# Kernel tuning notes

Measured on AMD Instinct MI355X. Metric: run time of the kernel, lower is better.

## Reference

```python
import jax, jax.numpy as jnp
import numpy as np

N, E, D, H = 50000, 800000, 128, 4

def setup_inputs() -> dict:
    key = jax.random.key(0)
    ks = jax.random.split(key, 6)
    x = jax.random.normal(ks[0], (N, D), dtype=jnp.float32)
    edge_index = jax.random.randint(ks[1], (2, E), 0, N, dtype=jnp.int64)
    W = jax.random.normal(ks[2], (D, H * D), dtype=jnp.float32) * (1.0 / np.sqrt(D))
    att_src = jax.random.normal(ks[3], (H, D), dtype=jnp.float32) * 0.1
    att_dst = jax.random.normal(ks[4], (H, D), dtype=jnp.float32) * 0.1
    bias = jnp.zeros((D,), dtype=jnp.float32)
    gamma = jnp.ones((D,), dtype=jnp.float32)
    beta = jnp.zeros((D,), dtype=jnp.float32)
    return {"x": x, "edge_index": edge_index, "W": W, "att_src": att_src,
            "att_dst": att_dst, "bias": bias, "gamma": gamma, "beta": beta}

def reference(x, edge_index, W, att_src, att_dst, bias, gamma, beta):
    src, dst = edge_index[0], edge_index[1]
    # GATConv: linear transform per head -> [N, H, D]
    xw = (x @ W).reshape(N, H, D)
    a_src = jnp.einsum('nhd,hd->nh', xw, att_src)  # [N, H]
    a_dst = jnp.einsum('nhd,hd->nh', xw, att_dst)  # [N, H]
    alpha = a_src[src] + a_dst[dst]                # [E, H]
    alpha = jax.nn.leaky_relu(alpha, negative_slope=0.2)
    # segment softmax over incoming edges of each dst node
    m = jax.ops.segment_max(alpha, dst, num_segments=N)   # [N, H]
    ex = jnp.exp(alpha - m[dst])                            # [E, H]
    denom = jax.ops.segment_sum(ex, dst, num_segments=N)   # [N, H]
    attn = ex / denom[dst]                                  # [E, H]
    msg = xw[src] * attn[:, :, None]                        # [E, H, D]
    agg = jax.ops.segment_sum(msg, dst, num_segments=N)    # [N, H, D]
    out = agg.mean(axis=1) + bias                           # concat=False: mean heads
    # LayerNorm (eps=1e-5)
    mu = out.mean(axis=-1, keepdims=True)
    var = out.var(axis=-1, keepdims=True)
    out = (out - mu) * jax.lax.rsqrt(var + 1e-5) * gamma + beta
    out = jax.nn.gelu(out, approximate=False)
    return out + x  # project is Identity (in_channels == out_channels)
```

## Files before the change

### kernel.cpp

```cpp
#include <hip/hip_runtime.h>
#include <hip/hip_bf16.h>
#include <hip/hip_fp16.h>
#include <math.h>

#define ND 128
#define NH 4
#define HD 512

typedef __attribute__((ext_vector_type(8))) short bf16x8;
typedef __attribute__((ext_vector_type(4))) float f32x4;
typedef __attribute__((ext_vector_type(2))) float f32x2;

__device__ __forceinline__ unsigned pack_bf16(float a, float b) {
    unsigned ua = __float_as_uint(a), ub = __float_as_uint(b);
    ua = (ua + 0x7fffu + ((ua >> 16) & 1u)) >> 16;
    ub = (ub + 0x7fffu + ((ub >> 16) & 1u)) >> 16;
    return ua | (ub << 16);
}
__device__ __forceinline__ unsigned short bf16r(float a) {
    unsigned ua = __float_as_uint(a);
    return (unsigned short)((ua + 0x7fffu + ((ua >> 16) & 1u)) >> 16);
}
__device__ __forceinline__ float bflo(unsigned u) { return __uint_as_float(u << 16); }
__device__ __forceinline__ float bfhi(unsigned u) { return __uint_as_float(u & 0xffff0000u); }
__device__ __forceinline__ unsigned pack_half2(float a, float b) {
    __half ha = __float2half(a), hb = __float2half(b);
    return (unsigned)__half_as_ushort(ha) | ((unsigned)__half_as_ushort(hb) << 16);
}
__device__ __forceinline__ float2 h22f(unsigned u) {
    __half2 h = *(__half2*)&u;
    return __half22float2(h);
}

__global__ __launch_bounds__(256) void prep_misc(const float* __restrict__ W,
                                                 const float* __restrict__ att_src,
                                                 const float* __restrict__ att_dst,
                                                 unsigned short* __restrict__ Ws,
                                                 float* __restrict__ pt,
                                                 const int* __restrict__ dst,
                                                 int* __restrict__ cnt, int ne) {
    int b = blockIdx.x;
    if (b < 16) {
        __shared__ float tile[64][65];
        int h = b >> 2, rt = (b >> 1) & 1, ct = b & 1;
        int tx = threadIdx.x;
        int rr = tx >> 6, c = tx & 63;
#pragma unroll
        for (int i = 0; i < 16; ++i) {
            int r = i * 4 + rr;
            tile[r][c] = W[(size_t)(rt * 64 + r) * HD + h * ND + ct * 64 + c];
        }
        __syncthreads();
#pragma unroll
        for (int i = 0; i < 16; ++i) {
            int r = i * 4 + rr;
            Ws[(size_t)(ct * 64 + r) * HD + h * ND + rt * 64 + c] = bf16r(tile[c][r]);
        }
    } else if (b < 48) {
        int w = threadIdx.x >> 6, lane = threadIdx.x & 63;
        int k = (b - 16) * 4 + w;
#pragma unroll
        for (int h = 0; h < NH; ++h) {
            float2 wv = ((const float2*)(W + (size_t)k * HD + h * ND))[lane];
            float2 as = ((const float2*)(att_src + h * ND))[lane];
            float2 ad = ((const float2*)(att_dst + h * ND))[lane];
            float ps = wv.x * as.x + wv.y * as.y;
            float pd = wv.x * ad.x + wv.y * ad.y;
#pragma unroll
            for (int off = 1; off < 64; off <<= 1) {
                ps += __shfl_xor(ps, off);
                pd += __shfl_xor(pd, off);
            }
            if (lane == 0) {
                pt[h * ND + k] = ps;
                pt[(4 + h) * ND + k] = pd;
            }
        }
    } else {
        int e = (b - 48) * 256 + threadIdx.x;
        if (e < ne) atomicAdd(&cnt[dst[e]], 1);
    }
}

__global__ __launch_bounds__(256) void ka_scanA(const float* __restrict__ x,
                                                const float* __restrict__ pt,
                                                unsigned* __restrict__ xb,
                                                float* __restrict__ a_src,
                                                float* __restrict__ a_dst,
                                                const int* __restrict__ cnt,
                                                int* __restrict__ partial,
                                                int* __restrict__ bsum,
                                                int n, int nbA) {
    __shared__ float pl[8 * ND];
    __shared__ int sh[256];
    if ((int)blockIdx.x < nbA) {
        { int t = threadIdx.x; ((float4*)pl)[t] = ((const float4*)pt)[t]; }
        __syncthreads();
        int wave = (blockIdx.x * 256 + threadIdx.x) >> 6;
        int lane = threadIdx.x & 63;
        if (wave >= n) return;
        float2 xv = ((const float2*)(x + (size_t)wave * ND))[lane];
        xb[(size_t)wave * 64 + lane] = pack_bf16(xv.x, xv.y);
#pragma unroll
        for (int o = 0; o < 8; ++o) {
            float2 pv = ((const float2*)(pl + o * ND))[lane];
            float v = xv.x * pv.x + xv.y * pv.y;
#pragma unroll
            for (int off = 1; off < 64; off <<= 1) v += __shfl_xor(v, off);
            if (lane == 0) {
                if (o < 4) a_src[(size_t)wave * NH + o] = v;
                else       a_dst[(size_t)wave * NH + (o - 4)] = v;
            }
        }
    } else {
        int bid = blockIdx.x - nbA;
        int gid = bid * 256 + threadIdx.x;
        int v = (gid < n) ? cnt[gid] : 0;
        int val = v;
        sh[threadIdx.x] = val;
        __syncthreads();
#pragma unroll
        for (int off = 1; off < 256; off <<= 1) {
            int add = (threadIdx.x >= off) ? sh[threadIdx.x - off] : 0;
            __syncthreads();
            val += add;
            sh[threadIdx.x] = val;
            __syncthreads();
        }
        if (gid < n) partial[gid] = val - v;
        if (threadIdx.x == 255) bsum[bid] = val;
    }
}

__global__ __launch_bounds__(256) void scanBC(const int* __restrict__ partial,
                                              const int* __restrict__ bsum,
                                              int* __restrict__ starts,
                                              int* __restrict__ cursor,
                                              int n, int ne, int nb) {
    __shared__ int sh[256];
    int t = threadIdx.x;
    int v = (t < nb) ? bsum[t] : 0;
    int val = v;
    sh[t] = val;
    __syncthreads();
#pragma unroll
    for (int off = 1; off < 256; off <<= 1) {
        int add = (t >= off) ? sh[t - off] : 0;
        __syncthreads();
        val += add;
        sh[t] = val;
        __syncthreads();
    }
    int myoff = (blockIdx.x == 0) ? 0 : sh[blockIdx.x - 1];
    int gid = blockIdx.x * 256 + t;
    if (gid < n) {
        int s = partial[gid] + myoff;
        starts[gid] = s;
        cursor[gid] = s;
    }
    if (gid == 0) starts[n] = ne;
}

__global__ __launch_bounds__(256) void scatter_edges_w(const int* __restrict__ src,
                                                       const int* __restrict__ dst,
                                                       const float* __restrict__ a_src,
                                                       const float* __restrict__ a_dst,
                                                       int* __restrict__ cursor,
                                                       uint4* __restrict__ eperm, int ne) {
    int e = blockIdx.x * 256 + threadIdx.x;
    if (e < ne) {
        int s = src[e], t = dst[e];
        float4 as = *(const float4*)(a_src + (size_t)s * NH);
        float4 ad = *(const float4*)(a_dst + (size_t)t * NH);
        float A0 = as.x + ad.x, A1 = as.y + ad.y, A2 = as.z + ad.z, A3 = as.w + ad.w;
        A0 = (A0 > 0.f) ? A0 : 0.2f * A0;
        A1 = (A1 > 0.f) ? A1 : 0.2f * A1;
        A2 = (A2 > 0.f) ? A2 : 0.2f * A2;
        A3 = (A3 > 0.f) ? A3 : 0.2f * A3;
        float e0 = __expf(A0), e1 = __expf(A1), e2 = __expf(A2), e3 = __expf(A3);
        int pos = atomicAdd(&cursor[t], 1);
        uint4 ev;
        ev.x = (unsigned)s;
        ev.y = pack_half2(e0, e1);
        ev.z = pack_half2(e2, e3);
        ev.w = 0u;
        eperm[pos] = ev;
    }
}

#define PK8()                                                              \
    { f32x2 xlo = {bflo(xv.x), bfhi(xv.x)};                                \
      f32x2 xhi = {bflo(xv.y), bfhi(xv.y)};                                \
      acc2[0] += xlo * w01.x; acc2[1] += xhi * w01.x;                      \
      acc2[2] += xlo * w01.y; acc2[3] += xhi * w01.y;                      \
      acc2[4] += xlo * w23.x; acc2[5] += xhi * w23.x;                      \
      acc2[6] += xlo * w23.y; acc2[7] += xhi * w23.y; }

__global__ __launch_bounds__(256) void node_agg(const uint4* __restrict__ eperm,
                                                const int* __restrict__ starts,
                                                const uint2* __restrict__ xb2,
                                                unsigned* __restrict__ u, int n) {
    int node = (blockIdx.x * 256 + threadIdx.x) >> 6;
    int lane = threadIdx.x & 63;
    if (node >= n) return;
    const int slot = lane & 31;
    const int half = lane >> 5;

    int s0 = starts[node], s1 = starts[node + 1];

    float den0 = 0.f, den1 = 0.f, den2 = 0.f, den3 = 0.f;
    f32x2 acc2[8];
#pragma unroll
    for (int j = 0; j < 8; ++j) acc2[j] = (f32x2){0.f, 0.f};

    for (int base = s0; base < s1; base += 16) {
        int rem = s1 - base; if (rem > 16) rem = 16;
        uint4 ev = {0u, 0u, 0u, 0u};
        if (lane < rem) ev = eperm[base + lane];
        {
            float2 dl = h22f(ev.y), dh = h22f(ev.z);
            den0 += dl.x; den1 += dl.y; den2 += dh.x; den3 += dh.y;
        }
        if (rem == 16) {
#pragma unroll
            for (int pp = 0; pp < 8; ++pp) {
                int j2 = 2 * pp + half;
                int s = __shfl((int)ev.x, j2);
                unsigned uy = __shfl(ev.y, j2);
                unsigned uz = __shfl(ev.z, j2);
                uint2 xv = xb2[(size_t)s * 32 + slot];
                float2 w01 = h22f(uy), w23 = h22f(uz);
                PK8();
            }
        } else {
            for (int jj = 0; jj < rem; jj += 2) {
                int j2 = jj + half;
                bool valid = (j2 < rem);
                int j2c = valid ? j2 : jj;
                int s = __shfl((int)ev.x, j2c);
                unsigned uy = __shfl(ev.y, j2c);
                unsigned uz = __shfl(ev.z, j2c);
                uint2 xv = xb2[(size_t)s * 32 + slot];
                float2 w01 = h22f(uy), w23 = h22f(uz);
                float m = valid ? 1.f : 0.f;
                w01.x *= m; w01.y *= m; w23.x *= m; w23.y *= m;
                PK8();
            }
        }
    }

#pragma unroll
    for (int off = 1; off < 64; off <<= 1) {
        den0 += __shfl_xor(den0, off);
        den1 += __shfl_xor(den1, off);
        den2 += __shfl_xor(den2, off);
        den3 += __shfl_xor(den3, off);
    }
    float i0 = (den0 > 0.f) ? 0.25f / den0 : 0.f;
    float i1 = (den1 > 0.f) ? 0.25f / den1 : 0.f;
    float i2 = (den2 > 0.f) ? 0.25f / den2 : 0.f;
    float i3 = (den3 > 0.f) ? 0.25f / den3 : 0.f;

    float v[16];
#pragma unroll
    for (int hh4 = 0; hh4 < 4; ++hh4) {
        float ih = (hh4 == 0) ? i0 : (hh4 == 1) ? i1 : (hh4 == 2) ? i2 : i3;
        v[hh4 * 4 + 0] = acc2[hh4 * 2].x * ih;
        v[hh4 * 4 + 1] = acc2[hh4 * 2].y * ih;
        v[hh4 * 4 + 2] = acc2[hh4 * 2 + 1].x * ih;
        v[hh4 * 4 + 3] = acc2[hh4 * 2 + 1].y * ih;
    }
#pragma unroll
    for (int j = 0; j < 16; ++j) v[j] += __shfl_xor(v[j], 32);

#pragma unroll
    for (int hh = 0; hh < 2; ++hh) {
        int h = half * 2 + hh;
        uint2 val;
        val.x = pack_bf16(v[h * 4 + 0], v[h * 4 + 1]);
        val.y = pack_bf16(v[h * 4 + 2], v[h * 4 + 3]);
        ((uint2*)u)[(size_t)node * 128 + h * 32 + slot] = val;
    }
}

__global__ __launch_bounds__(256) void gemm_out(
        const unsigned short* __restrict__ u, const unsigned short* __restrict__ Ws,
        const float* __restrict__ x, const float* __restrict__ bias,
        const float* __restrict__ gamma, const float* __restrict__ beta,
        float* __restrict__ out, int n) {
    __shared__ char Bs[32768];
    const int t = threadIdx.x;
    const int w = t >> 6, l = t & 63;
    const int e16 = l & 15, g16 = l >> 4;
    const int row0 = blockIdx.x * 128;

    int ar0 = row0 + w * 32 + e16;      if (ar0 >= n) ar0 = n - 1;
    int ar1 = row0 + w * 32 + 16 + e16; if (ar1 >= n) ar1 = n - 1;
    const unsigned short* ap0 = u + (size_t)ar0 * HD + g16 * 8;
    const unsigned short* ap1 = u + (size_t)ar1 * HD + g16 * 8;

    f32x4 acc[2][8];
#pragma unroll
    for (int mt = 0; mt < 2; ++mt)
#pragma unroll
        for (int nr = 0; nr < 8; ++nr) acc[mt][nr] = (f32x4){0.f, 0.f, 0.f, 0.f};

    const int swz = (e16 & 7) << 4;
    for (int kc = 0; kc < 4; ++kc) {
        if (kc) __syncthreads();
#pragma unroll
        for (int i = 0; i < 8; ++i) {
            int c = t + i * 256;
            int nl = c >> 4, kb = c & 15;
            uint4 pv = *(const uint4*)(Ws + (size_t)nl * HD + kc * 128 + kb * 8);
            *(uint4*)(Bs + nl * 256 + ((kb * 16) ^ ((nl & 7) << 4))) = pv;
        }
        __syncthreads();

#pragma unroll
        for (int ks = 0; ks < 4; ++ks) {
            int koff = (ks * 64 + g16 * 16) ^ swz;
            bf16x8 a0 = *(const bf16x8*)(ap0 + kc * 128 + ks * 32);
            bf16x8 a1 = *(const bf16x8*)(ap1 + kc * 128 + ks * 32);
#pragma unroll
            for (int nr = 0; nr < 8; ++nr) {
                bf16x8 b = *(const bf16x8*)(Bs + (nr * 16 + e16) * 256 + koff);
                acc[0][nr] = __builtin_amdgcn_mfma_f32_16x16x32_bf16(a0, b, acc[0][nr], 0, 0, 0);
                acc[1][nr] = __builtin_amdgcn_mfma_f32_16x16x32_bf16(a1, b, acc[1][nr], 0, 0, 0);
            }
        }
    }

    float bias_l[8], gam_l[8], bet_l[8];
#pragma unroll
    for (int c = 0; c < 8; ++c) {
        bias_l[c] = bias[c * 16 + e16];
        gam_l[c]  = gamma[c * 16 + e16];
        bet_l[c]  = beta[c * 16 + e16];
    }
#pragma unroll
    for (int mt = 0; mt < 2; ++mt) {
#pragma unroll
        for (int ri = 0; ri < 4; ++ri) {
            int grow = row0 + w * 32 + mt * 16 + g16 * 4 + ri;
            float val[8];
            float s = 0.f, s2 = 0.f;
#pragma unroll
            for (int c = 0; c < 8; ++c) {
                val[c] = acc[mt][c][ri] + bias_l[c];
                s += val[c]; s2 += val[c] * val[c];
            }
#pragma unroll
            for (int off = 1; off < 16; off <<= 1) {
                s += __shfl_xor(s, off);
                s2 += __shfl_xor(s2, off);
            }
            float mu = s * (1.0f / ND);
            float var = fmaxf(s2 * (1.0f / ND) - mu * mu, 0.0f);
            float inv = rsqrtf(var + 1e-5f);
            if (grow < n) {
#pragma unroll
                for (int c = 0; c < 8; ++c) {
                    float y = (val[c] - mu) * inv * gam_l[c] + bet_l[c];
                    y = 0.5f * y * (1.0f + erff(y * 0.70710678118654752f));
                    out[(size_t)grow * ND + c * 16 + e16] =
                        y + x[(size_t)grow * ND + c * 16 + e16];
                }
            }
        }
    }
}

extern "C" void kernel_launch(void* const* d_in, const int* in_sizes, int n_in,
                              void* d_out, int out_size, void* d_ws, size_t ws_size,
                              hipStream_t stream) {
    const float* x       = (const float*)d_in[0];
    const int*   edge    = (const int*)d_in[1];
    const float* W       = (const float*)d_in[2];
    const float* att_src = (const float*)d_in[3];
    const float* att_dst = (const float*)d_in[4];
    const float* bias    = (const float*)d_in[5];
    const float* gamma   = (const float*)d_in[6];
    const float* beta    = (const float*)d_in[7];
    float* out = (float*)d_out;

    const int n  = in_sizes[0] / ND;
    const int ne = in_sizes[1] / 2;
    const int* src = edge;
    const int* dst = edge + ne;

    const int nb  = (n + 255) / 256;
    const int nbA = (n + 3) / 4;

    char* wsp = (char*)d_ws;
    unsigned* xb        = (unsigned*)wsp;        wsp += (size_t)n * 64 * sizeof(unsigned);
    unsigned short* u   = (unsigned short*)wsp;  wsp += (size_t)n * HD * sizeof(short);
    unsigned short* Ws  = (unsigned short*)wsp;  wsp += (size_t)ND * HD * sizeof(short);
    float* pt      = (float*)wsp;               wsp += (size_t)8 * ND * sizeof(float);
    float* a_src   = (float*)wsp;               wsp += (size_t)n * NH * sizeof(float);
    float* a_dst   = (float*)wsp;               wsp += (size_t)n * NH * sizeof(float);
    uint4* eperm   = (uint4*)wsp;               wsp += (size_t)ne * sizeof(uint4);
    int*   cnt     = (int*)wsp;                 wsp += (size_t)n * sizeof(int);
    int*   partial = (int*)wsp;                 wsp += (size_t)n * sizeof(int);
    int*   bsum    = (int*)wsp;                 wsp += 256 * sizeof(int);
    int*   starts  = (int*)wsp;                 wsp += (size_t)(n + 1) * sizeof(int);
    int*   cursor  = (int*)wsp;                 wsp += (size_t)n * sizeof(int);

    (void)hipMemsetAsync(cnt, 0, (size_t)n * sizeof(int), stream);

    prep_misc<<<48 + (ne + 255) / 256, 256, 0, stream>>>(W, att_src, att_dst,
                                                         Ws, pt, dst, cnt, ne);

    ka_scanA<<<nbA + nb, 256, 0, stream>>>(x, pt, xb, a_src, a_dst,
                                           cnt, partial, bsum, n, nbA);

    scanBC<<<nb, 256, 0, stream>>>(partial, bsum, starts, cursor, n, ne, nb);

    scatter_edges_w<<<(ne + 255) / 256, 256, 0, stream>>>(src, dst, a_src, a_dst,
                                                          cursor, eperm, ne);

    node_agg<<<(n + 3) / 4, 256, 0, stream>>>(eperm, starts, (const uint2*)xb,
                                              (unsigned*)u, n);

    gemm_out<<<(n + 127) / 128, 256, 0, stream>>>(u, Ws, x, bias, gamma, beta, out, n);
}
```

Measured before the change: 217.8 us.

## Stage edge records in LDS and prefetch W tiles in registers for GEMM

```diff
diff --git a/kernel.cpp b/kernel.cpp
--- a/kernel.cpp
+++ b/kernel.cpp
@@ -200,7 +200,9 @@
                                                 const int* __restrict__ starts,
                                                 const uint2* __restrict__ xb2,
                                                 unsigned* __restrict__ u, int n) {
-    int node = (blockIdx.x * 256 + threadIdx.x) >> 6;
+    __shared__ uint4 estage[4][16];
+    const int w = threadIdx.x >> 6;
+    int node = blockIdx.x * 4 + w;
     int lane = threadIdx.x & 63;
     if (node >= n) return;
     const int slot = lane & 31;
@@ -217,6 +219,7 @@
         int rem = s1 - base; if (rem > 16) rem = 16;
         uint4 ev = {0u, 0u, 0u, 0u};
         if (lane < rem) ev = eperm[base + lane];
+        if (lane < 16) estage[w][lane] = ev;
         {
             float2 dl = h22f(ev.y), dh = h22f(ev.z);
             den0 += dl.x; den1 += dl.y; den2 += dh.x; den3 += dh.y;
@@ -224,24 +227,18 @@
         if (rem == 16) {
 #pragma unroll
             for (int pp = 0; pp < 8; ++pp) {
-                int j2 = 2 * pp + half;
-                int s = __shfl((int)ev.x, j2);
-                unsigned uy = __shfl(ev.y, j2);
-                unsigned uz = __shfl(ev.z, j2);
-                uint2 xv = xb2[(size_t)s * 32 + slot];
-                float2 w01 = h22f(uy), w23 = h22f(uz);
+                uint4 e2 = estage[w][2 * pp + half];
+                uint2 xv = xb2[(size_t)e2.x * 32 + slot];
+                float2 w01 = h22f(e2.y), w23 = h22f(e2.z);
                 PK8();
             }
         } else {
             for (int jj = 0; jj < rem; jj += 2) {
                 int j2 = jj + half;
                 bool valid = (j2 < rem);
-                int j2c = valid ? j2 : jj;
-                int s = __shfl((int)ev.x, j2c);
-                unsigned uy = __shfl(ev.y, j2c);
-                unsigned uz = __shfl(ev.z, j2c);
-                uint2 xv = xb2[(size_t)s * 32 + slot];
-                float2 w01 = h22f(uy), w23 = h22f(uz);
+                uint4 e2 = estage[w][valid ? j2 : jj];
+                uint2 xv = xb2[(size_t)e2.x * 32 + slot];
+                float2 w01 = h22f(e2.y), w23 = h22f(e2.z);
                 float m = valid ? 1.f : 0.f;
                 w01.x *= m; w01.y *= m; w23.x *= m; w23.y *= m;
                 PK8();
@@ -293,12 +290,18 @@
     const int w = t >> 6, l = t & 63;
     const int e16 = l & 15, g16 = l >> 4;
     const int row0 = blockIdx.x * 128;
+    const int snl = t >> 4, skb = t & 15;
 
     int ar0 = row0 + w * 32 + e16;      if (ar0 >= n) ar0 = n - 1;
     int ar1 = row0 + w * 32 + 16 + e16; if (ar1 >= n) ar1 = n - 1;
     const unsigned short* ap0 = u + (size_t)ar0 * HD + g16 * 8;
     const unsigned short* ap1 = u + (size_t)ar1 * HD + g16 * 8;
 
+    uint4 bpre[8];
+#pragma unroll
+    for (int i = 0; i < 8; ++i)
+        bpre[i] = *(const uint4*)(Ws + (size_t)(snl + i * 16) * HD + skb * 8);
+
     f32x4 acc[2][8];
 #pragma unroll
     for (int mt = 0; mt < 2; ++mt)
@@ -307,13 +310,16 @@
 
     const int swz = (e16 & 7) << 4;
     for (int kc = 0; kc < 4; ++kc) {
-        if (kc) __syncthreads();
 #pragma unroll
         for (int i = 0; i < 8; ++i) {
-            int c = t + i * 256;
-            int nl = c >> 4, kb = c & 15;
-            uint4 pv = *(const uint4*)(Ws + (size_t)nl * HD + kc * 128 + kb * 8);
-            *(uint4*)(Bs + nl * 256 + ((kb * 16) ^ ((nl & 7) << 4))) = pv;
+            int nl2 = snl + i * 16;
+            *(uint4*)(Bs + nl2 * 256 + ((skb * 16) ^ ((nl2 & 7) << 4))) = bpre[i];
+        }
+        if (kc < 3) {
+#pragma unroll
+            for (int i = 0; i < 8; ++i)
+                bpre[i] = *(const uint4*)(Ws + (size_t)(snl + i * 16) * HD
+                                          + (kc + 1) * 128 + skb * 8);
         }
         __syncthreads();
 
@@ -329,6 +335,7 @@
                 acc[1][nr] = __builtin_amdgcn_mfma_f32_16x16x32_bf16(a1, b, acc[1][nr], 0, 0, 0);
             }
         }
+        __syncthreads();
     }
 
     float bias_l[8], gam_l[8], bet_l[8];
```

Measured after the change: 232.9 us. +6.9%, slower.

## Use MFMA for per-node weighted aggregation via LDS-transposed neighbor tiles

Applied to the files above, without the earlier changes.

```diff
diff --git a/kernel.cpp b/kernel.cpp
--- a/kernel.cpp
+++ b/kernel.cpp
@@ -9,7 +9,6 @@
 
 typedef __attribute__((ext_vector_type(8))) short bf16x8;
 typedef __attribute__((ext_vector_type(4))) float f32x4;
-typedef __attribute__((ext_vector_type(2))) float f32x2;
 
 __device__ __forceinline__ unsigned pack_bf16(float a, float b) {
     unsigned ua = __float_as_uint(a), ub = __float_as_uint(b);
@@ -23,14 +22,6 @@
 }
 __device__ __forceinline__ float bflo(unsigned u) { return __uint_as_float(u << 16); }
 __device__ __forceinline__ float bfhi(unsigned u) { return __uint_as_float(u & 0xffff0000u); }
-__device__ __forceinline__ unsigned pack_half2(float a, float b) {
-    __half ha = __float2half(a), hb = __float2half(b);
-    return (unsigned)__half_as_ushort(ha) | ((unsigned)__half_as_ushort(hb) << 16);
-}
-__device__ __forceinline__ float2 h22f(unsigned u) {
-    __half2 h = *(__half2*)&u;
-    return __half22float2(h);
-}
 
 __global__ __launch_bounds__(256) void prep_misc(const float* __restrict__ W,
                                                  const float* __restrict__ att_src,
@@ -181,71 +172,70 @@
         int pos = atomicAdd(&cursor[t], 1);
         uint4 ev;
         ev.x = (unsigned)s;
-        ev.y = pack_half2(e0, e1);
-        ev.z = pack_half2(e2, e3);
+        ev.y = pack_bf16(e0, e1);
+        ev.z = pack_bf16(e2, e3);
         ev.w = 0u;
         eperm[pos] = ev;
     }
 }
 
-#define PK8()                                                              \
-    { f32x2 xlo = {bflo(xv.x), bfhi(xv.x)};                                \
-      f32x2 xhi = {bflo(xv.y), bfhi(xv.y)};                                \
-      acc2[0] += xlo * w01.x; acc2[1] += xhi * w01.x;                      \
-      acc2[2] += xlo * w01.y; acc2[3] += xhi * w01.y;                      \
-      acc2[4] += xlo * w23.x; acc2[5] += xhi * w23.x;                      \
-      acc2[6] += xlo * w23.y; acc2[7] += xhi * w23.y; }
-
 __global__ __launch_bounds__(256) void node_agg(const uint4* __restrict__ eperm,
                                                 const int* __restrict__ starts,
-                                                const uint2* __restrict__ xb2,
+                                                const unsigned* __restrict__ xb,
                                                 unsigned* __restrict__ u, int n) {
-    int node = (blockIdx.x * 256 + threadIdx.x) >> 6;
-    int lane = threadIdx.x & 63;
+    __shared__ char ldsb[4 * 6400];
+    const int w = threadIdx.x >> 6;
+    const int lane = threadIdx.x & 63;
+    const int node = blockIdx.x * 2 + (w >> 1);
+    const int wh = w & 1;
+    char* xT = ldsb + w * 6400;
+    char* wT = xT + 5120;
     if (node >= n) return;
-    const int slot = lane & 31;
-    const int half = lane >> 5;
+
+    const int e16 = lane & 15, g = lane >> 4;
+    const char* xbb = (const char*)xb;
 
     int s0 = starts[node], s1 = starts[node + 1];
 
     float den0 = 0.f, den1 = 0.f, den2 = 0.f, den3 = 0.f;
-    f32x2 acc2[8];
-#pragma unroll
-    for (int j = 0; j < 8; ++j) acc2[j] = (f32x2){0.f, 0.f};
-
-    for (int base = s0; base < s1; base += 16) {
-        int rem = s1 - base; if (rem > 16) rem = 16;
+    f32x4 acc[4];
+#pragma unroll
+    for (int b = 0; b < 4; ++b) acc[b] = (f32x4){0.f, 0.f, 0.f, 0.f};
+
+    for (int base = s0; base < s1; base += 32) {
+        int rem = s1 - base; if (rem > 32) rem = 32;
         uint4 ev = {0u, 0u, 0u, 0u};
         if (lane < rem) ev = eperm[base + lane];
-        {
-            float2 dl = h22f(ev.y), dh = h22f(ev.z);
-            den0 += dl.x; den1 += dl.y; den2 += dh.x; den3 += dh.y;
-        }
-        if (rem == 16) {
-#pragma unroll
-            for (int pp = 0; pp < 8; ++pp) {
-                int j2 = 2 * pp + half;
-                int s = __shfl((int)ev.x, j2);
-                unsigned uy = __shfl(ev.y, j2);
-                unsigned uz = __shfl(ev.z, j2);
-                uint2 xv = xb2[(size_t)s * 32 + slot];
-                float2 w01 = h22f(uy), w23 = h22f(uz);
-                PK8();
-            }
-        } else {
-            for (int jj = 0; jj < rem; jj += 2) {
-                int j2 = jj + half;
-                bool valid = (j2 < rem);
-                int j2c = valid ? j2 : jj;
-                int s = __shfl((int)ev.x, j2c);
-                unsigned uy = __shfl(ev.y, j2c);
-                unsigned uz = __shfl(ev.z, j2c);
-                uint2 xv = xb2[(size_t)s * 32 + slot];
-                float2 w01 = h22f(uy), w23 = h22f(uz);
-                float m = valid ? 1.f : 0.f;
-                w01.x *= m; w01.y *= m; w23.x *= m; w23.y *= m;
-                PK8();
-            }
+        den0 += bflo(ev.y); den1 += bfhi(ev.y);
+        den2 += bflo(ev.z); den3 += bfhi(ev.z);
+        if (lane < 32) {
+            *(unsigned short*)(wT + 0 * 80 + lane * 2) = (unsigned short)(ev.y & 0xffffu);
+            *(unsigned short*)(wT + 1 * 80 + lane * 2) = (unsigned short)(ev.y >> 16);
+            *(unsigned short*)(wT + 2 * 80 + lane * 2) = (unsigned short)(ev.z & 0xffffu);
+            *(unsigned short*)(wT + 3 * 80 + lane * 2) = (unsigned short)(ev.z >> 16);
+        }
+#pragma unroll
+        for (int i = 0; i < 4; ++i) {
+            int r = i * 8 + (lane >> 3);
+            int srcn = __shfl((int)ev.x, r);
+            uint4 pv = {0u, 0u, 0u, 0u};
+            if (r < rem)
+                pv = *(const uint4*)(xbb + (size_t)srcn * 256 + wh * 128 + (lane & 7) * 16);
+            char* bb = xT + ((lane & 7) >> 1) * 1280 + (((lane & 7) & 1) * 8) * 80 + r * 2;
+            *(unsigned short*)(bb + 0 * 80) = (unsigned short)(pv.x & 0xffffu);
+            *(unsigned short*)(bb + 1 * 80) = (unsigned short)(pv.x >> 16);
+            *(unsigned short*)(bb + 2 * 80) = (unsigned short)(pv.y & 0xffffu);
+            *(unsigned short*)(bb + 3 * 80) = (unsigned short)(pv.y >> 16);
+            *(unsigned short*)(bb + 4 * 80) = (unsigned short)(pv.z & 0xffffu);
+            *(unsigned short*)(bb + 5 * 80) = (unsigned short)(pv.z >> 16);
+            *(unsigned short*)(bb + 6 * 80) = (unsigned short)(pv.w & 0xffffu);
+            *(unsigned short*)(bb + 7 * 80) = (unsigned short)(pv.w >> 16);
+        }
+        bf16x8 Af = *(const bf16x8*)(wT + e16 * 80 + g * 16);
+#pragma unroll
+        for (int b = 0; b < 4; ++b) {
+            bf16x8 Bf = *(const bf16x8*)(xT + b * 1280 + e16 * 80 + g * 16);
+            acc[b] = __builtin_amdgcn_mfma_f32_16x16x32_bf16(Af, Bf, acc[b], 0, 0, 0);
         }
     }
 
@@ -256,30 +246,21 @@
         den2 += __shfl_xor(den2, off);
         den3 += __shfl_xor(den3, off);
     }
-    float i0 = (den0 > 0.f) ? 0.25f / den0 : 0.f;
-    float i1 = (den1 > 0.f) ? 0.25f / den1 : 0.f;
-    float i2 = (den2 > 0.f) ? 0.25f / den2 : 0.f;
-    float i3 = (den3 > 0.f) ? 0.25f / den3 : 0.f;
-
-    float v[16];
-#pragma unroll
-    for (int hh4 = 0; hh4 < 4; ++hh4) {
-        float ih = (hh4 == 0) ? i0 : (hh4 == 1) ? i1 : (hh4 == 2) ? i2 : i3;
-        v[hh4 * 4 + 0] = acc2[hh4 * 2].x * ih;
-        v[hh4 * 4 + 1] = acc2[hh4 * 2].y * ih;
-        v[hh4 * 4 + 2] = acc2[hh4 * 2 + 1].x * ih;
-        v[hh4 * 4 + 3] = acc2[hh4 * 2 + 1].y * ih;
-    }
-#pragma unroll
-    for (int j = 0; j < 16; ++j) v[j] += __shfl_xor(v[j], 32);
-
-#pragma unroll
-    for (int hh = 0; hh < 2; ++hh) {
-        int h = half * 2 + hh;
-        uint2 val;
-        val.x = pack_bf16(v[h * 4 + 0], v[h * 4 + 1]);
-        val.y = pack_bf16(v[h * 4 + 2], v[h * 4 + 3]);
-        ((uint2*)u)[(size_t)node * 128 + h * 32 + slot] = val;
+    float ih0 = (den0 > 0.f) ? 0.25f / den0 : 0.f;
+    float ih1 = (den1 > 0.f) ? 0.25f / den1 : 0.f;
+    float ih2 = (den2 > 0.f) ? 0.25f / den2 : 0.f;
+    float ih3 = (den3 > 0.f) ? 0.25f / den3 : 0.f;
+
+    if (g == 0) {
+        unsigned short* uu = (unsigned short*)u + (size_t)node * HD;
+#pragma unroll
+        for (int b = 0; b < 4; ++b) {
+            int dcol = wh * 64 + b * 16 + e16;
+            uu[0 * ND + dcol] = bf16r(acc[b][0] * ih0);
+            uu[1 * ND + dcol] = bf16r(acc[b][1] * ih1);
+            uu[2 * ND + dcol] = bf16r(acc[b][2] * ih2);
+            uu[3 * ND + dcol] = bf16r(acc[b][3] * ih3);
+        }
     }
 }
 
@@ -419,8 +400,7 @@
     scatter_edges_w<<<(ne + 255) / 256, 256, 0, stream>>>(src, dst, a_src, a_dst,
                                                           cursor, eperm, ne);
 
-    node_agg<<<(n + 3) / 4, 256, 0, stream>>>(eperm, starts, (const uint2*)xb,
-                                              (unsigned*)u, n);
+    node_agg<<<(n + 1) / 2, 256, 0, stream>>>(eperm, starts, xb, (unsigned*)u, n);
 
     gemm_out<<<(n + 127) / 128, 256, 0, stream>>>(u, Ws, x, bias, gamma, beta, out, n);
 }
```

New measurement: 282.4 us. +29.7%, slower.
